# Kernel optimization log

Hardware: AMD Instinct MI355X
Metric: run time of the kernel (lower is better)

## Reference

```python
import jax, jax.numpy as jnp
import numpy as np

NUM_HASHES = 10
GROUP = 2
K = 5


def _strip_att(x, conv_w, rvecs, horizontal):
    # x: [n, c, h, w]; conv_w: [group*k, c]; rvecs: [num_hashes, c]
    n, c, h, w = x.shape
    hw = h * w
    pad = K // 2

    # ---- LSH group selection (vectorized, no python batch loop) ----
    x_flat = x.reshape(n, c, hw).transpose(0, 2, 1)          # [n, hw, c]
    proj = jnp.einsum('ntc,hc->nth', x_flat, rvecs)          # [n, hw, num_hashes]
    codes = (proj > 0).astype(jnp.float32)
    pow2 = jnp.power(2.0, jnp.arange(NUM_HASHES, dtype=jnp.float32))
    dec = codes @ pow2                                       # [n, hw]
    order = jnp.argsort(dec, axis=1)                         # [n, hw]
    sorted_t = jnp.take_along_axis(x_flat, order[:, :, None], axis=1)  # [n, hw, c]

    # select_best_group: batch element with largest L2 norm, shared by all
    norms = jnp.linalg.norm(sorted_t.reshape(n, -1), axis=1)  # [n]
    best = jnp.argmax(norms)
    best_group = jnp.take(sorted_t, best, axis=0)             # [hw, c]
    bg = jnp.broadcast_to(best_group.T.reshape(1, c, h, w), (n, c, h, w))

    # ---- sigmoid-gated dynamic strip filter (1x1 conv) ----
    filt = jnp.einsum('oc,nchw->nohw', conv_w, bg)            # [n, group*K, h, w]
    filt = jax.nn.sigmoid(filt).reshape(n, GROUP, 1, K, hw)

    # ---- unfold (im2col) along the strip axis, reflect-padded ----
    if horizontal:
        xp = jnp.pad(x, ((0, 0), (0, 0), (0, 0), (pad, pad)), mode='reflect')
        windows = jnp.stack([xp[:, :, :, i:i + w] for i in range(K)], axis=2)  # [n,c,K,h,w]
    else:
        xp = jnp.pad(x, ((0, 0), (0, 0), (pad, pad), (0, 0)), mode='reflect')
        windows = jnp.stack([xp[:, :, i:i + h, :] for i in range(K)], axis=2)  # [n,c,K,h,w]
    xr = windows.reshape(n, GROUP, c // GROUP, K, hw)

    out = jnp.sum(xr * filt, axis=3).reshape(n, c, h, w)
    return out


def setup_inputs() -> dict:
    key = jax.random.key(0)
    ks = jax.random.split(key, 7)
    n, c, h, w = 4, 64, 256, 256
    return {
        'x': jax.random.normal(ks[0], (n, c, h, w), dtype=jnp.float32),
        'conv_h_w': jax.random.normal(ks[1], (GROUP * K, c), dtype=jnp.float32) * 0.1,
        'conv_w_w': jax.random.normal(ks[2], (GROUP * K, c), dtype=jnp.float32) * 0.1,
        'rvecs_h': jax.random.normal(ks[3], (NUM_HASHES, c), dtype=jnp.float32),
        'rvecs_w': jax.random.normal(ks[4], (NUM_HASHES, c), dtype=jnp.float32),
        'gamma': jax.random.normal(ks[5], (c,), dtype=jnp.float32),
        'beta': jax.random.normal(ks[6], (c,), dtype=jnp.float32),
    }


def reference(x, conv_h_w, conv_w_w, rvecs_h, rvecs_w, gamma, beta):
    out = _strip_att(x, conv_h_w, rvecs_h, horizontal=True)
    out = _strip_att(out, conv_w_w, rvecs_w, horizontal=False)
    return gamma[None, :, None, None] * out + x * beta[None, :, None, None]
```

## Files before the change

kernel.cpp:

```cpp
#include <hip/hip_runtime.h>

#define NB 4
#define C 64
#define H 256
#define W 256
#define HW (H * W)
#define NH 10
#define KK 5
#define NBINS 1024
#define CHUNK 256
#define NCHUNK (HW / CHUNK)

__global__ __launch_bounds__(256) void sumsq_kernel(const float* __restrict__ x,
                                                    float* __restrict__ part) {
    int bid = blockIdx.x;
    int b = bid >> 8, ch = bid & 255;
    const float4* p = reinterpret_cast<const float4*>(x + (size_t)b * C * HW) + (size_t)ch * 4096;
    float s = 0.f;
    for (int i = threadIdx.x; i < 4096; i += 256) {
        float4 v = p[i];
        s += v.x * v.x + v.y * v.y + v.z * v.z + v.w * v.w;
    }
    __shared__ float red[256];
    red[threadIdx.x] = s;
    __syncthreads();
    for (int off = 128; off; off >>= 1) {
        if (threadIdx.x < off) red[threadIdx.x] += red[threadIdx.x + off];
        __syncthreads();
    }
    if (threadIdx.x == 0) part[bid] = red[0];
}

__global__ __launch_bounds__(256) void hash_kernel(const float* __restrict__ Xall,
                                                   const float* __restrict__ part,
                                                   int per_batch,
                                                   const float* __restrict__ rvecs,
                                                   const float* __restrict__ cwg,
                                                   float* __restrict__ filtU,
                                                   int* __restrict__ dec,
                                                   int* __restrict__ hist) {
    __shared__ float tile[CHUNK][33];
    __shared__ float rv[NH * C];
    __shared__ float cw[NH * C];
    __shared__ int lhist[NBINS];
    __shared__ float4 red4[256];
    int t = threadIdx.x;
    for (int i = t; i < NH * C; i += 256) { rv[i] = rvecs[i]; cw[i] = cwg[i]; }
    for (int i = t; i < NBINS; i += 256) lhist[i] = 0;

    float4 ss = make_float4(0.f, 0.f, 0.f, 0.f);
    for (int i = t; i < per_batch; i += 256) {
        ss.x += part[0 * per_batch + i];
        ss.y += part[1 * per_batch + i];
        ss.z += part[2 * per_batch + i];
        ss.w += part[3 * per_batch + i];
    }
    red4[t] = ss;
    __syncthreads();
    for (int off = 128; off; off >>= 1) {
        if (t < off) {
            red4[t].x += red4[t + off].x;
            red4[t].y += red4[t + off].y;
            red4[t].z += red4[t + off].z;
            red4[t].w += red4[t + off].w;
        }
        __syncthreads();
    }
    float4 nm = red4[0];
    float nv[NB] = {nm.x, nm.y, nm.z, nm.w};
    int best = 0;
    float m = nv[0];
#pragma unroll
    for (int i = 1; i < NB; i++)
        if (nv[i] > m) { m = nv[i]; best = i; }

    const float* X = Xall + (size_t)best * C * HW;
    int p0 = blockIdx.x * CHUNK;
    float acc[NH], cacc[NH];
#pragma unroll
    for (int h2 = 0; h2 < NH; h2++) { acc[h2] = 0.f; cacc[h2] = 0.f; }

    for (int half = 0; half < 2; half++) {
        __syncthreads();
        for (int c = 0; c < 32; c++) tile[t][c] = X[(size_t)(half * 32 + c) * HW + p0 + t];
        __syncthreads();
        for (int c = 0; c < 32; c += 4) {
            float4 v = make_float4(tile[t][c], tile[t][c + 1], tile[t][c + 2], tile[t][c + 3]);
#pragma unroll
            for (int h2 = 0; h2 < NH; h2++) {
                const float* r = rv + h2 * C + half * 32 + c;
                const float* cc = cw + h2 * C + half * 32 + c;
                acc[h2] += v.x * r[0] + v.y * r[1] + v.z * r[2] + v.w * r[3];
                cacc[h2] += v.x * cc[0] + v.y * cc[1] + v.z * cc[2] + v.w * cc[3];
            }
        }
    }
    int d = 0;
#pragma unroll
    for (int h2 = 0; h2 < NH; h2++) d |= (acc[h2] > 0.f) ? (1 << h2) : 0;
    dec[p0 + t] = d;
    atomicAdd(&lhist[d], 1);

    float* fu = filtU + (size_t)(p0 + t) * 12;
    float s01 = 1.f / (1.f + expf(-cacc[0])), s1 = 1.f / (1.f + expf(-cacc[1]));
    float s2 = 1.f / (1.f + expf(-cacc[2])), s3 = 1.f / (1.f + expf(-cacc[3]));
    float s4 = 1.f / (1.f + expf(-cacc[4])), s5 = 1.f / (1.f + expf(-cacc[5]));
    float s6 = 1.f / (1.f + expf(-cacc[6])), s7 = 1.f / (1.f + expf(-cacc[7]));
    float s8 = 1.f / (1.f + expf(-cacc[8])), s9 = 1.f / (1.f + expf(-cacc[9]));
    *reinterpret_cast<float4*>(fu + 0) = make_float4(s01, s1, s2, s3);
    *reinterpret_cast<float4*>(fu + 4) = make_float4(s4, s5, s6, s7);
    *reinterpret_cast<float4*>(fu + 8) = make_float4(s8, s9, 0.f, 0.f);

    __syncthreads();
    for (int i = t; i < NBINS; i += 256) hist[(size_t)i * NCHUNK + blockIdx.x] = lhist[i];
}

__global__ __launch_bounds__(256) void scan1_kernel(int* __restrict__ hist,
                                                    int* __restrict__ bintot) {
    int t = threadIdx.x;
    int lane = t & 63;
    int b = blockIdx.x * 4 + (t >> 6);
    int4 v = *reinterpret_cast<int4*>(hist + (size_t)b * NCHUNK + lane * 4);
    int s0 = v.x;
    int s1 = s0 + v.y;
    int s2 = s1 + v.z;
    int s3 = s2 + v.w;
    int s = s3;
#pragma unroll
    for (int off = 1; off < 64; off <<= 1) {
        int nbr = __shfl_up(s, off);
        if (lane >= off) s += nbr;
    }
    int excl = s - s3;
    int4 o;
    o.x = excl;
    o.y = excl + s0;
    o.z = excl + s1;
    o.w = excl + s2;
    *reinterpret_cast<int4*>(hist + (size_t)b * NCHUNK + lane * 4) = o;
    if (lane == 63) bintot[b] = s;
}

__global__ __launch_bounds__(256) void scatter_kernel(const int* __restrict__ dec,
                                                      const int* __restrict__ hist,
                                                      const int* __restrict__ bintot,
                                                      int* __restrict__ order) {
    __shared__ int boffs[NBINS];
    __shared__ int wtot[4];
    __shared__ int keys[CHUNK];
    int t = threadIdx.x;
    int lane = t & 63;
    int w = t >> 6;
    int4 v = *reinterpret_cast<const int4*>(bintot + t * 4);
    int s0 = v.x, s1 = s0 + v.y, s2 = s1 + v.z, s3 = s2 + v.w;
    int s = s3;
#pragma unroll
    for (int off = 1; off < 64; off <<= 1) {
        int nbr = __shfl_up(s, off);
        if (lane >= off) s += nbr;
    }
    int excl = s - s3;
    if (lane == 63) wtot[w] = s;
    __syncthreads();
    int wbase = 0;
#pragma unroll
    for (int i = 0; i < 4; i++) wbase += (i < w) ? wtot[i] : 0;
    boffs[t * 4 + 0] = wbase + excl;
    boffs[t * 4 + 1] = wbase + excl + s0;
    boffs[t * 4 + 2] = wbase + excl + s1;
    boffs[t * 4 + 3] = wbase + excl + s2;

    int p0 = blockIdx.x * CHUNK;
    int k = dec[p0 + t];
    keys[t] = k;
    __syncthreads();
    int r = 0;
    for (int j = 0; j < t; j++) r += (keys[j] == k) ? 1 : 0;
    int dst = boffs[k] + hist[(size_t)k * NCHUNK + blockIdx.x] + r;
    order[dst] = p0 + t;
}

__global__ __launch_bounds__(256) void filtsig_kernel(const float* __restrict__ filtU,
                                                      const int* __restrict__ order,
                                                      float* __restrict__ filt) {
    int p = blockIdx.x * 256 + threadIdx.x;
    int orig = order[p];
    const float4* fu = reinterpret_cast<const float4*>(filtU + (size_t)orig * 12);
    float4 a = fu[0], b4 = fu[1], c4 = fu[2];
    float v[10] = {a.x, a.y, a.z, a.w, b4.x, b4.y, b4.z, b4.w, c4.x, c4.y};
#pragma unroll
    for (int h2 = 0; h2 < NH; h2++) filt[(size_t)h2 * HW + p] = v[h2];
}

__global__ __launch_bounds__(256) void convh_kernel(const float* __restrict__ X,
                                                    const float* __restrict__ filt,
                                                    float* __restrict__ out1,
                                                    float* __restrict__ part) {
    int bid = blockIdx.x;
    int rb = bid & 63;
    int c = (bid >> 6) & (C - 1);
    int n = bid >> 12;
    int g = c >> 5;
    int t = threadIdx.x;
    int x4 = (t & 63) * 4;
    int y = rb * 4 + (t >> 6);

    const float* src = X + (((size_t)n * C + c) * H + y) * W;
    float4 M = *reinterpret_cast<const float4*>(src + x4);
    float s0, s1, s6, s7;
    if (x4 > 0) {
        float4 L = *reinterpret_cast<const float4*>(src + x4 - 4);
        s0 = L.z; s1 = L.w;
    } else {
        s0 = M.z; s1 = M.y;
    }
    if (x4 < W - 4) {
        float4 R = *reinterpret_cast<const float4*>(src + x4 + 4);
        s6 = R.x; s7 = R.y;
    } else {
        s6 = M.z; s7 = M.y;
    }
    float s[8] = {s0, s1, M.x, M.y, M.z, M.w, s6, s7};

    const float* fb = filt + (size_t)g * KK * HW + (size_t)y * W + x4;
    float4 acc = make_float4(0.f, 0.f, 0.f, 0.f);
#pragma unroll
    for (int k = 0; k < KK; k++) {
        float4 f = *reinterpret_cast<const float4*>(fb + (size_t)k * HW);
        acc.x += s[k] * f.x;
        acc.y += s[k + 1] * f.y;
        acc.z += s[k + 2] * f.z;
        acc.w += s[k + 3] * f.w;
    }
    *reinterpret_cast<float4*>(out1 + (((size_t)n * C + c) * H + y) * W + x4) = acc;

    float ss = acc.x * acc.x + acc.y * acc.y + acc.z * acc.z + acc.w * acc.w;
#pragma unroll
    for (int off = 32; off; off >>= 1) ss += __shfl_down(ss, off);
    __shared__ float wred[4];
    if ((t & 63) == 0) wred[t >> 6] = ss;
    __syncthreads();
    if (t == 0) part[bid] = wred[0] + wred[1] + wred[2] + wred[3];
}

__global__ __launch_bounds__(256) void convv_kernel(const float* __restrict__ out1,
                                                    const float* __restrict__ filt,
                                                    const float* __restrict__ x,
                                                    const float* __restrict__ gamma,
                                                    const float* __restrict__ beta,
                                                    float* __restrict__ out) {
    int bid = blockIdx.x;
    int yc = bid & 3;
    int c = (bid >> 2) & (C - 1);
    int n = bid >> 8;
    int g = c >> 5;
    int t = threadIdx.x;
    int x4 = (t & 63) * 4;
    int ys = yc * 64 + (t >> 6) * 16;

    const float* plane = out1 + ((size_t)n * C + c) * HW;
    float4 win[KK];
#pragma unroll
    for (int i = 0; i < 4; i++) {
        int yy = ys - 2 + i;
        yy = yy < 0 ? -yy : yy;
        win[i] = *reinterpret_cast<const float4*>(plane + (size_t)yy * W + x4);
    }
    float gm = gamma[c], bt = beta[c];
    const float* fgb = filt + (size_t)g * KK * HW;
    for (int dy = 0; dy < 16; dy++) {
        int y = ys + dy;
        int yy = y + 2;
        yy = (yy >= H) ? (2 * H - 2 - yy) : yy;
        win[4] = *reinterpret_cast<const float4*>(plane + (size_t)yy * W + x4);
        const float* fb = fgb + (size_t)y * W + x4;
        float4 acc = make_float4(0.f, 0.f, 0.f, 0.f);
#pragma unroll
        for (int k = 0; k < KK; k++) {
            float4 f = *reinterpret_cast<const float4*>(fb + (size_t)k * HW);
            acc.x += win[k].x * f.x;
            acc.y += win[k].y * f.y;
            acc.z += win[k].z * f.z;
            acc.w += win[k].w * f.w;
        }
        size_t idx = (((size_t)n * C + c) * H + y) * W + x4;
        float4 xv = *reinterpret_cast<const float4*>(x + idx);
        float4 o;
        o.x = gm * acc.x + bt * xv.x;
        o.y = gm * acc.y + bt * xv.y;
        o.z = gm * acc.z + bt * xv.z;
        o.w = gm * acc.w + bt * xv.w;
        *reinterpret_cast<float4*>(out + idx) = o;
#pragma unroll
        for (int k = 0; k < 4; k++) win[k] = win[k + 1];
    }
}

extern "C" void kernel_launch(void* const* d_in, const int* in_sizes, int n_in,
                              void* d_out, int out_size, void* d_ws, size_t ws_size,
                              hipStream_t stream) {
    const float* x      = (const float*)d_in[0];
    const float* conv_h = (const float*)d_in[1];
    const float* conv_w = (const float*)d_in[2];
    const float* rv_h   = (const float*)d_in[3];
    const float* rv_w   = (const float*)d_in[4];
    const float* gamma  = (const float*)d_in[5];
    const float* beta   = (const float*)d_in[6];
    float* out = (float*)d_out;

    char* w = (char*)d_ws;
    size_t off = 0;
    float* out1   = (float*)(w + off); off += (size_t)NB * C * HW * 4;
    float* filtU  = (float*)(w + off); off += (size_t)HW * 12 * 4;
    float* filt   = (float*)(w + off); off += (size_t)NH * HW * 4;
    int*   dec    = (int*)  (w + off); off += (size_t)HW * 4;
    int*   order  = (int*)  (w + off); off += (size_t)HW * 4;
    int*   hist   = (int*)  (w + off); off += (size_t)NCHUNK * NBINS * 4;
    int*   bintot = (int*)  (w + off); off += 4096;
    float* part1  = (float*)(w + off); off += (size_t)NB * 256 * 4;
    float* part2  = (float*)(w + off); off += (size_t)NB * 4096 * 4;

    sumsq_kernel<<<NB * 256, 256, 0, stream>>>(x, part1);
    hash_kernel<<<NCHUNK, 256, 0, stream>>>(x, part1, 256, rv_h, conv_h, filtU, dec, hist);
    scan1_kernel<<<NBINS / 4, 256, 0, stream>>>(hist, bintot);
    scatter_kernel<<<NCHUNK, 256, 0, stream>>>(dec, hist, bintot, order);
    filtsig_kernel<<<HW / 256, 256, 0, stream>>>(filtU, order, filt);
    convh_kernel<<<NB * C * (H / 4), 256, 0, stream>>>(x, filt, out1, part2);

    hash_kernel<<<NCHUNK, 256, 0, stream>>>(out1, part2, 4096, rv_w, conv_w, filtU, dec, hist);
    scan1_kernel<<<NBINS / 4, 256, 0, stream>>>(hist, bintot);
    scatter_kernel<<<NCHUNK, 256, 0, stream>>>(dec, hist, bintot, order);
    filtsig_kernel<<<HW / 256, 256, 0, stream>>>(filtU, order, filt);
    convv_kernel<<<NB * C * (H / 64), 256, 0, stream>>>(out1, filt, x, gamma, beta, out);
}
```

Measured before the change: 151.5 us.

## Speculatively hash all batches while computing norms, fuse scatter with filter gather

Instead of first computing per-batch sum-of-squares and then hashing only the best batch, the hash kernel now processes every batch element in one pass. In the same pass it computes the sum of squares, the LSH code, the sigmoid filter and a per-batch histogram. The scan and scatter kernels then pick the best batch from the partials, and the scatter writes filter values directly to their sorted positions, which removes the order buffer and the separate filtsig kernel. The norm reduction epilogue is also dropped from convh. The cost is four times more hash compute and extra workspace for filtU, dec and hist, traded for a full read of x that is shared, fewer launches and fewer serial dependencies.

```diff
diff --git a/kernel.cpp b/kernel.cpp
--- a/kernel.cpp
+++ b/kernel.cpp
@@ -11,50 +11,72 @@
 #define CHUNK 256
 #define NCHUNK (HW / CHUNK)
 
-__global__ __launch_bounds__(256) void sumsq_kernel(const float* __restrict__ x,
-                                                    float* __restrict__ part) {
-    int bid = blockIdx.x;
-    int b = bid >> 8, ch = bid & 255;
-    const float4* p = reinterpret_cast<const float4*>(x + (size_t)b * C * HW) + (size_t)ch * 4096;
-    float s = 0.f;
-    for (int i = threadIdx.x; i < 4096; i += 256) {
-        float4 v = p[i];
-        s += v.x * v.x + v.y * v.y + v.z * v.z + v.w * v.w;
-    }
+__global__ __launch_bounds__(256) void spec_hash_kernel(const float* __restrict__ Xall,
+                                                        const float* __restrict__ rvecs,
+                                                        const float* __restrict__ cwg,
+                                                        float* __restrict__ part,
+                                                        float* __restrict__ filtU,
+                                                        int* __restrict__ dec,
+                                                        int* __restrict__ hist) {
+    __shared__ int lhist[NBINS];
     __shared__ float red[256];
-    red[threadIdx.x] = s;
+    int t = threadIdx.x;
+    int b = blockIdx.x >> 8;
+    int ch = blockIdx.x & (NCHUNK - 1);
+    int p0 = ch * CHUNK;
+    for (int i = t; i < NBINS; i += 256) lhist[i] = 0;
+
+    const float* X = Xall + (size_t)b * C * HW + p0 + t;
+    float acc[NH], cacc[NH];
+#pragma unroll
+    for (int h = 0; h < NH; h++) { acc[h] = 0.f; cacc[h] = 0.f; }
+    float ssq = 0.f;
+#pragma unroll 8
+    for (int i = 0; i < C; i++) {
+        float v = X[(size_t)i * HW];
+        ssq += v * v;
+#pragma unroll
+        for (int h = 0; h < NH; h++) {
+            acc[h] += v * rvecs[h * C + i];
+            cacc[h] += v * cwg[h * C + i];
+        }
+    }
+    int d = 0;
+#pragma unroll
+    for (int h = 0; h < NH; h++) d |= (acc[h] > 0.f) ? (1 << h) : 0;
+    dec[(size_t)b * HW + p0 + t] = d;
+
+    float* fu = filtU + ((size_t)b * HW + p0 + t) * 12;
+    float sg[NH];
+#pragma unroll
+    for (int h = 0; h < NH; h++) sg[h] = 1.f / (1.f + expf(-cacc[h]));
+    *reinterpret_cast<float4*>(fu + 0) = make_float4(sg[0], sg[1], sg[2], sg[3]);
+    *reinterpret_cast<float4*>(fu + 4) = make_float4(sg[4], sg[5], sg[6], sg[7]);
+    *reinterpret_cast<float4*>(fu + 8) = make_float4(sg[8], sg[9], 0.f, 0.f);
+
+    __syncthreads();
+    atomicAdd(&lhist[d], 1);
+    red[t] = ssq;
     __syncthreads();
     for (int off = 128; off; off >>= 1) {
-        if (threadIdx.x < off) red[threadIdx.x] += red[threadIdx.x + off];
+        if (t < off) red[t] += red[t + off];
         __syncthreads();
     }
-    if (threadIdx.x == 0) part[bid] = red[0];
-}
-
-__global__ __launch_bounds__(256) void hash_kernel(const float* __restrict__ Xall,
-                                                   const float* __restrict__ part,
-                                                   int per_batch,
-                                                   const float* __restrict__ rvecs,
-                                                   const float* __restrict__ cwg,
-                                                   float* __restrict__ filtU,
-                                                   int* __restrict__ dec,
-                                                   int* __restrict__ hist) {
-    __shared__ float tile[CHUNK][33];
-    __shared__ float rv[NH * C];
-    __shared__ float cw[NH * C];
-    __shared__ int lhist[NBINS];
+    if (t == 0) part[blockIdx.x] = red[0];
+    for (int i = t; i < NBINS; i += 256)
+        hist[((size_t)b * NBINS + i) * NCHUNK + ch] = lhist[i];
+}
+
+__global__ __launch_bounds__(256) void scan1_kernel(const float* __restrict__ part,
+                                                    int* __restrict__ hist,
+                                                    int* __restrict__ bintot) {
     __shared__ float4 red4[256];
     int t = threadIdx.x;
-    for (int i = t; i < NH * C; i += 256) { rv[i] = rvecs[i]; cw[i] = cwg[i]; }
-    for (int i = t; i < NBINS; i += 256) lhist[i] = 0;
-
-    float4 ss = make_float4(0.f, 0.f, 0.f, 0.f);
-    for (int i = t; i < per_batch; i += 256) {
-        ss.x += part[0 * per_batch + i];
-        ss.y += part[1 * per_batch + i];
-        ss.z += part[2 * per_batch + i];
-        ss.w += part[3 * per_batch + i];
-    }
+    float4 ss;
+    ss.x = part[0 * NCHUNK + t];
+    ss.y = part[1 * NCHUNK + t];
+    ss.z = part[2 * NCHUNK + t];
+    ss.w = part[3 * NCHUNK + t];
     red4[t] = ss;
     __syncthreads();
     for (int off = 128; off; off >>= 1) {
@@ -74,57 +96,11 @@
     for (int i = 1; i < NB; i++)
         if (nv[i] > m) { m = nv[i]; best = i; }
 
-    const float* X = Xall + (size_t)best * C * HW;
-    int p0 = blockIdx.x * CHUNK;
-    float acc[NH], cacc[NH];
-#pragma unroll
-    for (int h2 = 0; h2 < NH; h2++) { acc[h2] = 0.f; cacc[h2] = 0.f; }
-
-    for (int half = 0; half < 2; half++) {
-        __syncthreads();
-        for (int c = 0; c < 32; c++) tile[t][c] = X[(size_t)(half * 32 + c) * HW + p0 + t];
-        __syncthreads();
-        for (int c = 0; c < 32; c += 4) {
-            float4 v = make_float4(tile[t][c], tile[t][c + 1], tile[t][c + 2], tile[t][c + 3]);
-#pragma unroll
-            for (int h2 = 0; h2 < NH; h2++) {
-                const float* r = rv + h2 * C + half * 32 + c;
-                const float* cc = cw + h2 * C + half * 32 + c;
-                acc[h2] += v.x * r[0] + v.y * r[1] + v.z * r[2] + v.w * r[3];
-                cacc[h2] += v.x * cc[0] + v.y * cc[1] + v.z * cc[2] + v.w * cc[3];
-            }
-        }
-    }
-    int d = 0;
-#pragma unroll
-    for (int h2 = 0; h2 < NH; h2++) d |= (acc[h2] > 0.f) ? (1 << h2) : 0;
-    dec[p0 + t] = d;
-    atomicAdd(&lhist[d], 1);
-
-    float* fu = filtU + (size_t)(p0 + t) * 12;
-    float s01 = 1.f / (1.f + expf(-cacc[0])), s1 = 1.f / (1.f + expf(-cacc[1]));
-    float s2 = 1.f / (1.f + expf(-cacc[2])), s3 = 1.f / (1.f + expf(-cacc[3]));
-    float s4 = 1.f / (1.f + expf(-cacc[4])), s5 = 1.f / (1.f + expf(-cacc[5]));
-    float s6 = 1.f / (1.f + expf(-cacc[6])), s7 = 1.f / (1.f + expf(-cacc[7]));
-    float s8 = 1.f / (1.f + expf(-cacc[8])), s9 = 1.f / (1.f + expf(-cacc[9]));
-    *reinterpret_cast<float4*>(fu + 0) = make_float4(s01, s1, s2, s3);
-    *reinterpret_cast<float4*>(fu + 4) = make_float4(s4, s5, s6, s7);
-    *reinterpret_cast<float4*>(fu + 8) = make_float4(s8, s9, 0.f, 0.f);
-
-    __syncthreads();
-    for (int i = t; i < NBINS; i += 256) hist[(size_t)i * NCHUNK + blockIdx.x] = lhist[i];
-}
-
-__global__ __launch_bounds__(256) void scan1_kernel(int* __restrict__ hist,
-                                                    int* __restrict__ bintot) {
-    int t = threadIdx.x;
     int lane = t & 63;
-    int b = blockIdx.x * 4 + (t >> 6);
-    int4 v = *reinterpret_cast<int4*>(hist + (size_t)b * NCHUNK + lane * 4);
-    int s0 = v.x;
-    int s1 = s0 + v.y;
-    int s2 = s1 + v.z;
-    int s3 = s2 + v.w;
+    int bin = blockIdx.x * 4 + (t >> 6);
+    int* base = hist + ((size_t)best * NBINS + bin) * NCHUNK;
+    int4 v = *reinterpret_cast<int4*>(base + lane * 4);
+    int s0 = v.x, s1 = s0 + v.y, s2 = s1 + v.z, s3 = s2 + v.w;
     int s = s3;
 #pragma unroll
     for (int off = 1; off < 64; off <<= 1) {
@@ -137,18 +113,45 @@
     o.y = excl + s0;
     o.z = excl + s1;
     o.w = excl + s2;
-    *reinterpret_cast<int4*>(hist + (size_t)b * NCHUNK + lane * 4) = o;
-    if (lane == 63) bintot[b] = s;
-}
-
-__global__ __launch_bounds__(256) void scatter_kernel(const int* __restrict__ dec,
+    *reinterpret_cast<int4*>(base + lane * 4) = o;
+    if (lane == 63) bintot[bin] = s;
+}
+
+__global__ __launch_bounds__(256) void scatter_kernel(const float* __restrict__ part,
+                                                      const int* __restrict__ dec,
                                                       const int* __restrict__ hist,
                                                       const int* __restrict__ bintot,
-                                                      int* __restrict__ order) {
+                                                      const float* __restrict__ filtU,
+                                                      float* __restrict__ filt) {
+    __shared__ float4 red4[256];
     __shared__ int boffs[NBINS];
     __shared__ int wtot[4];
     __shared__ int keys[CHUNK];
     int t = threadIdx.x;
+    float4 ss;
+    ss.x = part[0 * NCHUNK + t];
+    ss.y = part[1 * NCHUNK + t];
+    ss.z = part[2 * NCHUNK + t];
+    ss.w = part[3 * NCHUNK + t];
+    red4[t] = ss;
+    __syncthreads();
+    for (int off = 128; off; off >>= 1) {
+        if (t < off) {
+            red4[t].x += red4[t + off].x;
+            red4[t].y += red4[t + off].y;
+            red4[t].z += red4[t + off].z;
+            red4[t].w += red4[t + off].w;
+        }
+        __syncthreads();
+    }
+    float4 nm = red4[0];
+    float nv[NB] = {nm.x, nm.y, nm.z, nm.w};
+    int best = 0;
+    float m = nv[0];
+#pragma unroll
+    for (int i = 1; i < NB; i++)
+        if (nv[i] > m) { m = nv[i]; best = i; }
+
     int lane = t & 63;
     int w = t >> 6;
     int4 v = *reinterpret_cast<const int4*>(bintot + t * 4);
@@ -171,31 +174,23 @@
     boffs[t * 4 + 3] = wbase + excl + s2;
 
     int p0 = blockIdx.x * CHUNK;
-    int k = dec[p0 + t];
+    int k = dec[(size_t)best * HW + p0 + t];
     keys[t] = k;
     __syncthreads();
     int r = 0;
     for (int j = 0; j < t; j++) r += (keys[j] == k) ? 1 : 0;
-    int dst = boffs[k] + hist[(size_t)k * NCHUNK + blockIdx.x] + r;
-    order[dst] = p0 + t;
-}
-
-__global__ __launch_bounds__(256) void filtsig_kernel(const float* __restrict__ filtU,
-                                                      const int* __restrict__ order,
-                                                      float* __restrict__ filt) {
-    int p = blockIdx.x * 256 + threadIdx.x;
-    int orig = order[p];
-    const float4* fu = reinterpret_cast<const float4*>(filtU + (size_t)orig * 12);
+    int dst = boffs[k] + hist[((size_t)best * NBINS + k) * NCHUNK + blockIdx.x] + r;
+
+    const float4* fu = reinterpret_cast<const float4*>(filtU + ((size_t)best * HW + p0 + t) * 12);
     float4 a = fu[0], b4 = fu[1], c4 = fu[2];
-    float v[10] = {a.x, a.y, a.z, a.w, b4.x, b4.y, b4.z, b4.w, c4.x, c4.y};
-#pragma unroll
-    for (int h2 = 0; h2 < NH; h2++) filt[(size_t)h2 * HW + p] = v[h2];
+    float vv[10] = {a.x, a.y, a.z, a.w, b4.x, b4.y, b4.z, b4.w, c4.x, c4.y};
+#pragma unroll
+    for (int h = 0; h < NH; h++) filt[(size_t)h * HW + dst] = vv[h];
 }
 
 __global__ __launch_bounds__(256) void convh_kernel(const float* __restrict__ X,
                                                     const float* __restrict__ filt,
-                                                    float* __restrict__ out1,
-                                                    float* __restrict__ part) {
+                                                    float* __restrict__ out1) {
     int bid = blockIdx.x;
     int rb = bid & 63;
     int c = (bid >> 6) & (C - 1);
@@ -233,14 +228,6 @@
         acc.w += s[k + 3] * f.w;
     }
     *reinterpret_cast<float4*>(out1 + (((size_t)n * C + c) * H + y) * W + x4) = acc;
-
-    float ss = acc.x * acc.x + acc.y * acc.y + acc.z * acc.z + acc.w * acc.w;
-#pragma unroll
-    for (int off = 32; off; off >>= 1) ss += __shfl_down(ss, off);
-    __shared__ float wred[4];
-    if ((t & 63) == 0) wred[t >> 6] = ss;
-    __syncthreads();
-    if (t == 0) part[bid] = wred[0] + wred[1] + wred[2] + wred[3];
 }
 
 __global__ __launch_bounds__(256) void convv_kernel(const float* __restrict__ out1,
@@ -311,25 +298,21 @@
     char* w = (char*)d_ws;
     size_t off = 0;
     float* out1   = (float*)(w + off); off += (size_t)NB * C * HW * 4;
-    float* filtU  = (float*)(w + off); off += (size_t)HW * 12 * 4;
+    float* filtU  = (float*)(w + off); off += (size_t)NB * HW * 12 * 4;
     float* filt   = (float*)(w + off); off += (size_t)NH * HW * 4;
-    int*   dec    = (int*)  (w + off); off += (size_t)HW * 4;
-    int*   order  = (int*)  (w + off); off += (size_t)HW * 4;
-    int*   hist   = (int*)  (w + off); off += (size_t)NCHUNK * NBINS * 4;
+    int*   dec    = (int*)  (w + off); off += (size_t)NB * HW * 4;
+    int*   hist   = (int*)  (w + off); off += (size_t)NB * NBINS * NCHUNK * 4;
     int*   bintot = (int*)  (w + off); off += 4096;
-    float* part1  = (float*)(w + off); off += (size_t)NB * 256 * 4;
-    float* part2  = (float*)(w + off); off += (size_t)NB * 4096 * 4;
-
-    sumsq_kernel<<<NB * 256, 256, 0, stream>>>(x, part1);
-    hash_kernel<<<NCHUNK, 256, 0, stream>>>(x, part1, 256, rv_h, conv_h, filtU, dec, hist);
-    scan1_kernel<<<NBINS / 4, 256, 0, stream>>>(hist, bintot);
-    scatter_kernel<<<NCHUNK, 256, 0, stream>>>(dec, hist, bintot, order);
-    filtsig_kernel<<<HW / 256, 256, 0, stream>>>(filtU, order, filt);
-    convh_kernel<<<NB * C * (H / 4), 256, 0, stream>>>(x, filt, out1, part2);
-
-    hash_kernel<<<NCHUNK, 256, 0, stream>>>(out1, part2, 4096, rv_w, conv_w, filtU, dec, hist);
-    scan1_kernel<<<NBINS / 4, 256, 0, stream>>>(hist, bintot);
-    scatter_kernel<<<NCHUNK, 256, 0, stream>>>(dec, hist, bintot, order);
-    filtsig_kernel<<<HW / 256, 256, 0, stream>>>(filtU, order, filt);
-    convv_kernel<<<NB * C * (H / 64), 256, 0, stream>>>(out1, filt, x, gamma, beta, out);
-}
+    float* part1  = (float*)(w + off); off += (size_t)NB * NCHUNK * 4;
+    float* part2  = (float*)(w + off); off += (size_t)NB * NCHUNK * 4;
+
+    spec_hash_kernel<<<NB * NCHUNK, 256, 0, stream>>>(x, rv_h, conv_h, part1, filtU, dec, hist);
+    scan1_kernel<<<NBINS / 4, 256, 0, stream>>>(part1, hist, bintot);
+    scatter_kernel<<<NCHUNK, 256, 0, stream>>>(part1, dec, hist, bintot, filtU, filt);
+    convh_kernel<<<NB * C * (H / 4), 256, 0, stream>>>(x, filt, out1);
+
+    spec_hash_kernel<<<NB * NCHUNK, 256, 0, stream>>>(out1, rv_w, conv_w, part2, filtU, dec, hist);
+    scan1_kernel<<<NBINS / 4, 256, 0, stream>>>(part2, hist, bintot);
+    scatter_kernel<<<NCHUNK, 256, 0, stream>>>(part2, dec, hist, bintot, filtU, filt);
+    convv_kernel<<<NB * C * 4, 256, 0, stream>>>(out1, filt, x, gamma, beta, out);
+}
```

New measurement: 158.6 us. 1.05x slower.
